# Performance work log

Hardware: AMD Instinct MI355X
Metric: run time of the kernel (lower is better)

The kernel has to match this reference:

```python
import jax, jax.numpy as jnp
import numpy as np

B, S, E = 2, 2048, 2048
H, KV, D = 16, 4, 128
G = H // KV  # query heads per kv head
THETA = 10000.0


def setup_inputs() -> dict:
    key = jax.random.key(0)
    ks = jax.random.split(key, 5)
    scale = 0.02
    return {
        "x": jax.random.normal(ks[0], (B, S, E), dtype=jnp.float32),
        "Wq": jax.random.normal(ks[1], (E, H * D), dtype=jnp.float32) * scale,
        "Wk": jax.random.normal(ks[2], (E, KV * D), dtype=jnp.float32) * scale,
        "Wv": jax.random.normal(ks[3], (E, KV * D), dtype=jnp.float32) * scale,
        "Wo": jax.random.normal(ks[4], (E, E), dtype=jnp.float32) * scale,
    }


def _rope_tables(seq_len, head_dim, theta):
    inv_freq = 1.0 / theta ** (jnp.arange(0, head_dim, 2, dtype=jnp.float32) / head_dim)
    t = jnp.arange(seq_len, dtype=jnp.float32)
    freqs = jnp.outer(t, inv_freq)  # [S, D/2]
    cos = jnp.concatenate([jnp.cos(freqs), jnp.cos(freqs)], axis=-1)  # [S, D]
    sin = jnp.concatenate([jnp.sin(freqs), jnp.sin(freqs)], axis=-1)
    return cos, sin


def _apply_rope(x, cos, sin):
    # x: [B, h, S, D]; cos/sin: [S, D] broadcast over batch/heads
    d2 = x.shape[-1] // 2
    x1, x2 = x[..., :d2], x[..., d2:]
    rotated = jnp.concatenate([-x2, x1], axis=-1)
    return x * cos + rotated * sin


def reference(x, Wq, Wk, Wv, Wo):
    b, s, _ = x.shape
    q = (x @ Wq).reshape(b, s, H, D).transpose(0, 2, 1, 3)   # [B,H,S,D]
    k = (x @ Wk).reshape(b, s, KV, D).transpose(0, 2, 1, 3)  # [B,KV,S,D]
    v = (x @ Wv).reshape(b, s, KV, D).transpose(0, 2, 1, 3)

    cos, sin = _rope_tables(s, D, THETA)
    q = _apply_rope(q, cos, sin)
    k = _apply_rope(k, cos, sin)

    # GQA: q head h attends to kv head h // G (repeat_interleave order)
    qg = q.reshape(b, KV, G, s, D)
    scores = jnp.einsum("bkgsd,bktd->bkgst", qg, k) / jnp.sqrt(jnp.asarray(D, x.dtype))
    causal = jnp.tril(jnp.ones((s, s), dtype=bool))
    scores = jnp.where(causal, scores, jnp.asarray(-jnp.inf, scores.dtype))
    attn = jax.nn.softmax(scores, axis=-1)
    out = jnp.einsum("bkgst,bktd->bkgsd", attn, v)  # [B,KV,G,S,D]
    out = out.reshape(b, H, s, D).transpose(0, 2, 1, 3).reshape(b, s, H * D)
    return out @ Wo
```

## Files before the change

### kernel.cpp

```cpp
#include <hip/hip_runtime.h>
#include <stdint.h>

#define B_ 2
#define S_ 2048
#define E_ 2048
#define H_ 16
#define KV_ 4
#define D_ 128
#define G_ (H_ / KV_)
#define M_ (B_ * S_)
#define NQKV 3072

typedef unsigned short u16;
typedef unsigned int u32;
typedef __bf16 bf16x8 __attribute__((ext_vector_type(8)));
typedef float f32x4 __attribute__((ext_vector_type(4)));

__device__ __forceinline__ u16 f2bf(float f) {
  __bf16 h = (__bf16)f;
  return *(u16*)&h;
}
__device__ __forceinline__ float bf2f(u16 x) {
  return __uint_as_float(((u32)x) << 16);
}

__device__ __forceinline__ void gload_lds16(const u16* g, u16* lds) {
  __builtin_amdgcn_global_load_lds((const __attribute__((address_space(1))) u32*)g,
                                   (__attribute__((address_space(3))) u32*)lds,
                                   16, 0, 0);
}

__global__ __launch_bounds__(256) void build_trig(float2* __restrict__ tbl) {
  int i = blockIdx.x * 256 + threadIdx.x;
  if (i >= S_ * 64) return;
  int d = i & 63, s = i >> 6;
  float ang = (float)s * expf(-0.14391156831212787f * (float)d);
  float sn, cs;
  sincosf(ang, &sn, &cs);
  tbl[i] = make_float2(cs, sn);
}

__global__ __launch_bounds__(256) void convert_fp32_bf16(const float4* __restrict__ x,
                                                         uint2* __restrict__ o, int n4) {
  int i = blockIdx.x * 256 + threadIdx.x;
  if (i >= n4) return;
  float4 v = x[i];
  uint2 r;
  r.x = (u32)f2bf(v.x) | ((u32)f2bf(v.y) << 16);
  r.y = (u32)f2bf(v.z) | ((u32)f2bf(v.w) << 16);
  o[i] = r;
}

__global__ __launch_bounds__(256) void transpose_conv_all(const float* __restrict__ Wq,
                                                          const float* __restrict__ Wk,
                                                          const float* __restrict__ Wv,
                                                          const float* __restrict__ Wo,
                                                          u16* __restrict__ WqT,
                                                          u16* __restrict__ WkT,
                                                          u16* __restrict__ WvT,
                                                          u16* __restrict__ WoT) {
  __shared__ float tile[32][33];
  int bx = blockIdx.x;
  const float* W;
  u16* Wt;
  int Ndim, nx;
  if (bx < 64)       { W = Wq; Wt = WqT; Ndim = 2048; nx = bx; }
  else if (bx < 80)  { W = Wk; Wt = WkT; Ndim = 512;  nx = bx - 64; }
  else if (bx < 96)  { W = Wv; Wt = WvT; Ndim = 512;  nx = bx - 80; }
  else               { W = Wo; Wt = WoT; Ndim = 2048; nx = bx - 96; }
  int n0 = nx * 32, k0 = blockIdx.y * 32;
  int tx = threadIdx.x, ty = threadIdx.y;
#pragma unroll
  for (int i = 0; i < 4; i++) {
    int r = ty + i * 8;
    tile[r][tx] = W[(size_t)(k0 + r) * Ndim + n0 + tx];
  }
  __syncthreads();
#pragma unroll
  for (int i = 0; i < 4; i++) {
    int r = ty + i * 8;
    Wt[(size_t)(n0 + r) * 2048 + k0 + tx] = f2bf(tile[tx][r]);
  }
}

__global__ __launch_bounds__(256) void transpose_v(const u16* __restrict__ QKV,
                                                   u16* __restrict__ Vt) {
  __shared__ u16 tile[32][33];
  int bkv = blockIdx.z;
  int b = bkv / KV_, kv = bkv % KV_;
  int s0 = blockIdx.x * 32, d0 = blockIdx.y * 32;
  int tx = threadIdx.x, ty = threadIdx.y;
#pragma unroll
  for (int i = 0; i < 4; i++) {
    int r = ty + i * 8;
    tile[r][tx] = QKV[(size_t)(b * S_ + s0 + r) * NQKV + 2560 + kv * D_ + d0 + tx];
  }
  __syncthreads();
#pragma unroll
  for (int i = 0; i < 4; i++) {
    int r = ty + i * 8;
    Vt[((size_t)(b * KV_ + kv) * D_ + d0 + r) * S_ + s0 + tx] = tile[tx][r];
  }
}

__global__ __launch_bounds__(256) void rope_k_repack(const u16* __restrict__ QKV,
                                                     u16* __restrict__ Kp,
                                                     const float2* __restrict__ tbl,
                                                     int total) {
  int idx = blockIdx.x * 256 + threadIdx.x;
  if (idx >= total) return;
  int d = idx & 63;
  int rem = idx >> 6;
  int kv = rem & (KV_ - 1);
  int row = rem >> 2;
  int b = row >> 11;
  int spos = row & (S_ - 1);
  size_t src = (size_t)row * NQKV + 2048 + kv * D_ + d;
  float x0 = bf2f(QKV[src]);
  float x1 = bf2f(QKV[src + 64]);
  float2 t = tbl[(spos << 6) + d];
  size_t dst = ((size_t)((b * KV_ + kv) * S_ + spos)) * D_ + d;
  Kp[dst]      = f2bf(x0 * t.x - x1 * t.y);
  Kp[dst + 64] = f2bf(x1 * t.x + x0 * t.y);
}

__global__ __launch_bounds__(256) void rope_q_inplace(u16* __restrict__ QKV,
                                                      const float2* __restrict__ tbl,
                                                      int total) {
  int idx = blockIdx.x * 256 + threadIdx.x;
  if (idx >= total) return;
  int d = idx & 63;
  int rem = idx >> 6;
  int h = rem & (H_ - 1);
  int row = rem >> 4;
  int spos = row & (S_ - 1);
  size_t base = (size_t)row * NQKV + h * D_ + d;
  float x0 = bf2f(QKV[base]);
  float x1 = bf2f(QKV[base + 64]);
  float2 t = tbl[(spos << 6) + d];
  const float scale = 0.08838834764831845f;
  QKV[base]      = f2bf((x0 * t.x - x1 * t.y) * scale);
  QKV[base + 64] = f2bf((x1 * t.x + x0 * t.y) * scale);
}

__global__ __launch_bounds__(512, 2) void gemm256x192_qkv(const u16* __restrict__ A,
                                                          const u16* __restrict__ Bt,
                                                          u16* __restrict__ C) {
  extern __shared__ __align__(16) u16 smem[];
  const int Kdim = 2048;
  const int m0 = blockIdx.y * 256, n0 = blockIdx.x * 192;
  const int tid  = threadIdx.x;
  const int lane = tid & 63;
  const int wave = tid >> 6;
  const int wm   = wave >> 2;
  const int wn   = wave & 3;
  const int quad = lane >> 4, lm = lane & 15;

  int soffA[2], sldbA[2];
#pragma unroll
  for (int i = 0; i < 2; i++) {
    int cc  = i * 512 + tid;
    int row = cc >> 3;
    int q   = (cc & 7) ^ (row & 7);
    soffA[i] = row * Kdim + q * 8;
    sldbA[i] = (i * 512 + wave * 64) * 8;
  }
  const int rowB = tid >> 3;
  const int soffB = rowB * Kdim + (((tid & 7) ^ (rowB & 7)) * 8);
  const int sldbB = wave * 512;
  auto STAGE_A = [&](const u16* g, u16* l) {
    gload_lds16(g + soffA[0], l + sldbA[0]);
    gload_lds16(g + soffA[1], l + sldbA[1]);
  };
  auto STAGE_B = [&](const u16* g, u16* l) {
    gload_lds16(g + soffB, l + sldbB);
  };

  int cs0 = ((0 + quad) ^ (lm & 7)) * 8;
  int cs1 = ((4 + quad) ^ (lm & 7)) * 8;

  const u16* Ag = A  + (size_t)m0 * Kdim;
  const u16* Bg = Bt + (size_t)n0 * Kdim;
  const size_t hstepA = (size_t)128 * Kdim;
  const size_t tstepB = (size_t)64 * Kdim;

  f32x4 acc[8][3];
  f32x4 zero = {0.f, 0.f, 0.f, 0.f};
#pragma unroll
  for (int m = 0; m < 8; m++)
#pragma unroll
    for (int n = 0; n < 3; n++) acc[m][n] = zero;

  int bthird[3], brow[3];
#pragma unroll
  for (int nt = 0; nt < 3; nt++) {
    int R = wn * 48 + nt * 16;
    bthird[nt] = R >> 6;
    brow[nt] = (R & 63) + lm;
  }

  const int NKT = Kdim >> 6;

  STAGE_B(Bg,                    smem + 32768 + 0 * 4096);
  STAGE_A(Ag,                    smem + 0 * 8192);
  STAGE_A(Ag + hstepA,           smem + 1 * 8192);
  STAGE_B(Bg + tstepB,           smem + 32768 + 1 * 4096);
  STAGE_B(Bg + 2 * tstepB,       smem + 32768 + 2 * 4096);
  STAGE_B(Bg + 64,               smem + 32768 + 3 * 4096);
  STAGE_A(Ag + 64,               smem + 2 * 8192);
  STAGE_A(Ag + hstepA + 64,      smem + 3 * 8192);
  asm volatile("s_waitcnt vmcnt(5)" ::: "memory");
  __builtin_amdgcn_s_barrier();

  for (int kt = 0; kt < NKT; ++kt) {
    const int cur = kt & 1;
    const u16* regA  = smem + (cur * 2 + wm) * 8192;
    const u16* regB3 = smem + 32768 + cur * 3 * 4096;
    bf16x8 af[4][2], bf[3][2];

#pragma unroll
    for (int nt = 0; nt < 3; nt++) {
      const u16* p = regB3 + bthird[nt] * 4096 + brow[nt] * 64;
      bf[nt][0] = *(const bf16x8*)(p + cs0);
      bf[nt][1] = *(const bf16x8*)(p + cs1);
    }
#pragma unroll
    for (int m = 0; m < 4; m++) {
      af[m][0] = *(const bf16x8*)(regA + (m * 16 + lm) * 64 + cs0);
      af[m][1] = *(const bf16x8*)(regA + (m * 16 + lm) * 64 + cs1);
    }
    if (kt + 1 < NKT) {
      const u16* bn = Bg + (size_t)(kt + 1) * 64;
      u16* sb = smem + 32768 + ((cur ^ 1) * 3) * 4096;
      STAGE_B(bn + tstepB,     sb + 1 * 4096);
      STAGE_B(bn + 2 * tstepB, sb + 2 * 4096);
    }
    asm volatile("s_waitcnt lgkmcnt(0)" ::: "memory");
    __builtin_amdgcn_s_barrier();
    __builtin_amdgcn_s_setprio(1);
#pragma unroll
    for (int m = 0; m < 4; m++)
#pragma unroll
      for (int n = 0; n < 2; n++) {
        acc[m][n] = __builtin_amdgcn_mfma_f32_16x16x32_bf16(af[m][0], bf[n][0], acc[m][n], 0, 0, 0);
        acc[m][n] = __builtin_amdgcn_mfma_f32_16x16x32_bf16(af[m][1], bf[n][1], acc[m][n], 0, 0, 0);
      }
    __builtin_amdgcn_s_setprio(0);
    __builtin_amdgcn_s_barrier();

    if (kt + 2 < NKT)
      STAGE_B(Bg + (size_t)(kt + 2) * 64, smem + 32768 + (cur * 3 + 0) * 4096);
    __builtin_amdgcn_s_barrier();
    __builtin_amdgcn_s_setprio(1);
#pragma unroll
    for (int m = 0; m < 4; m++) {
      acc[m][2] = __builtin_amdgcn_mfma_f32_16x16x32_bf16(af[m][0], bf[2][0], acc[m][2], 0, 0, 0);
      acc[m][2] = __builtin_amdgcn_mfma_f32_16x16x32_bf16(af[m][1], bf[2][1], acc[m][2], 0, 0, 0);
    }
    __builtin_amdgcn_s_setprio(0);
    __builtin_amdgcn_s_barrier();

#pragma unroll
    for (int m = 0; m < 4; m++) {
      af[m][0] = *(const bf16x8*)(regA + ((m + 4) * 16 + lm) * 64 + cs0);
      af[m][1] = *(const bf16x8*)(regA + ((m + 4) * 16 + lm) * 64 + cs1);
    }
    asm volatile("s_waitcnt lgkmcnt(0)" ::: "memory");
    __builtin_amdgcn_s_barrier();
    __builtin_amdgcn_s_setprio(1);
#pragma unroll
    for (int m = 0; m < 4; m++)
#pragma unroll
      for (int n = 0; n < 2; n++) {
        acc[m + 4][n] = __builtin_amdgcn_mfma_f32_16x16x32_bf16(af[m][0], bf[n][0], acc[m + 4][n], 0, 0, 0);
        acc[m + 4][n] = __builtin_amdgcn_mfma_f32_16x16x32_bf16(af[m][1], bf[n][1], acc[m + 4][n], 0, 0, 0);
      }
    __builtin_amdgcn_s_setprio(0);
    __builtin_amdgcn_s_barrier();

    if (kt + 2 < NKT) {
      STAGE_A(Ag + (size_t)(kt + 2) * 64,          smem + (cur * 2 + 0) * 8192);
      STAGE_A(Ag + hstepA + (size_t)(kt + 2) * 64, smem + (cur * 2 + 1) * 8192);
    }
    __builtin_amdgcn_s_setprio(1);
#pragma unroll
    for (int m = 0; m < 4; m++) {
      acc[m + 4][2] = __builtin_amdgcn_mfma_f32_16x16x32_bf16(af[m][0], bf[2][0], acc[m + 4][2], 0, 0, 0);
      acc[m + 4][2] = __builtin_amdgcn_mfma_f32_16x16x32_bf16(af[m][1], bf[2][1], acc[m + 4][2], 0, 0, 0);
    }
    __builtin_amdgcn_s_setprio(0);
    asm volatile("s_waitcnt vmcnt(5)" ::: "memory");
    __builtin_amdgcn_s_barrier();
  }

#pragma unroll
  for (int m = 0; m < 8; m++) {
    const int row = m0 + wm * 128 + m * 16 + quad * 4;
#pragma unroll
    for (int n = 0; n < 3; n++) {
      const int col = n0 + wn * 48 + n * 16 + lm;
#pragma unroll
      for (int r = 0; r < 4; r++)
        C[(size_t)(row + r) * NQKV + col] = f2bf(acc[m][n][r]);
    }
  }
}

__global__ __launch_bounds__(512, 2) void gemm256x128_wo(const u16* __restrict__ A,
                                                         const u16* __restrict__ Bt,
                                                         float* __restrict__ C) {
  extern __shared__ __align__(16) u16 smem[];
  const int Kdim = 2048, Ndim = 2048;
  const int m0 = blockIdx.y * 256, n0 = blockIdx.x * 128;
  const int tid  = threadIdx.x;
  const int lane = tid & 63;
  const int wave = tid >> 6;
  const int wm   = wave >> 2;
  const int wn   = wave & 3;
  const int bh   = wn >> 1;
  const int nb   = (wn & 1) * 32;
  const int quad = lane >> 4, lm = lane & 15;

  int soffA[2], sldbA[2];
#pragma unroll
  for (int i = 0; i < 2; i++) {
    int cc  = i * 512 + tid;
    int row = cc >> 3;
    int q   = (cc & 7) ^ (row & 7);
    soffA[i] = row * Kdim + q * 8;
    sldbA[i] = (i * 512 + wave * 64) * 8;
  }
  const int rowB = tid >> 3;
  const int soffB = rowB * Kdim + (((tid & 7) ^ (rowB & 7)) * 8);
  const int sldbB = wave * 512;
  auto STAGE_A = [&](const u16* g, u16* l) {
    gload_lds16(g + soffA[0], l + sldbA[0]);
    gload_lds16(g + soffA[1], l + sldbA[1]);
  };
  auto STAGE_B = [&](const u16* g, u16* l) {
    gload_lds16(g + soffB, l + sldbB);
  };

  int cs0 = ((0 + quad) ^ (lm & 7)) * 8;
  int cs1 = ((4 + quad) ^ (lm & 7)) * 8;

  const u16* Ag = A  + (size_t)m0 * Kdim;
  const u16* Bg = Bt + (size_t)n0 * Kdim;
  const size_t hstepA = (size_t)128 * Kdim;
  const size_t hstepB = (size_t)64 * Kdim;

  f32x4 acc[8][2];
  f32x4 zero = {0.f, 0.f, 0.f, 0.f};
#pragma unroll
  for (int m = 0; m < 8; m++) {
    acc[m][0] = zero;
    acc[m][1] = zero;
  }

  const int NKT = Kdim >> 6;

  STAGE_B(Bg,              smem + 32768 + 0 * 4096);
  STAGE_A(Ag,              smem + 0 * 8192);
  STAGE_A(Ag + hstepA,     smem + 1 * 8192);
  STAGE_B(Bg + hstepB,     smem + 32768 + 1 * 4096);
  STAGE_B(Bg + 64,         smem + 32768 + 2 * 4096);
  STAGE_A(Ag + 64,         smem + 2 * 8192);
  STAGE_A(Ag + hstepA + 64, smem + 3 * 8192);
  asm volatile("s_waitcnt vmcnt(5)" ::: "memory");
  __builtin_amdgcn_s_barrier();

  for (int kt = 0; kt < NKT; ++kt) {
    const int cur = kt & 1;
    const u16* regA = smem + (cur * 2 + wm) * 8192;
    const u16* regB = smem + 32768 + (cur * 2 + bh) * 4096;
    bf16x8 af[4][2], bf[2][2];

#pragma unroll
    for (int n = 0; n < 2; n++) {
      bf[n][0] = *(const bf16x8*)(regB + (nb + n * 16 + lm) * 64 + cs0);
      bf[n][1] = *(const bf16x8*)(regB + (nb + n * 16 + lm) * 64 + cs1);
    }
#pragma unroll
    for (int m = 0; m < 4; m++) {
      af[m][0] = *(const bf16x8*)(regA + (m * 16 + lm) * 64 + cs0);
      af[m][1] = *(const bf16x8*)(regA + (m * 16 + lm) * 64 + cs1);
    }
    if (kt + 1 < NKT)
      STAGE_B(Bg + hstepB + (size_t)(kt + 1) * 64,
              smem + 32768 + (((kt + 1) & 1) * 2 + 1) * 4096);
    asm volatile("s_waitcnt lgkmcnt(0)" ::: "memory");
    __builtin_amdgcn_s_barrier();
    __builtin_amdgcn_s_setprio(1);
#pragma unroll
    for (int m = 0; m < 2; m++)
#pragma unroll
      for (int n = 0; n < 2; n++) {
        acc[m][n] = __builtin_amdgcn_mfma_f32_16x16x32_bf16(af[m][0], bf[n][0], acc[m][n], 0, 0, 0);
        acc[m][n] = __builtin_amdgcn_mfma_f32_16x16x32_bf16(af[m][1], bf[n][1], acc[m][n], 0, 0, 0);
      }
    __builtin_amdgcn_s_setprio(0);
    __builtin_amdgcn_s_barrier();

    if (kt + 2 < NKT)
      STAGE_B(Bg + (size_t)(kt + 2) * 64, smem + 32768 + (cur * 2 + 0) * 4096);
    __builtin_amdgcn_s_barrier();
    __builtin_amdgcn_s_setprio(1);
#pragma unroll
    for (int m = 2; m < 4; m++)
#pragma unroll
      for (int n = 0; n < 2; n++) {
        acc[m][n] = __builtin_amdgcn_mfma_f32_16x16x32_bf16(af[m][0], bf[n][0], acc[m][n], 0, 0, 0);
        acc[m][n] = __builtin_amdgcn_mfma_f32_16x16x32_bf16(af[m][1], bf[n][1], acc[m][n], 0, 0, 0);
      }
    __builtin_amdgcn_s_setprio(0);
    __builtin_amdgcn_s_barrier();

#pragma unroll
    for (int m = 0; m < 4; m++) {
      af[m][0] = *(const bf16x8*)(regA + ((m + 4) * 16 + lm) * 64 + cs0);
      af[m][1] = *(const bf16x8*)(regA + ((m + 4) * 16 + lm) * 64 + cs1);
    }
    asm volatile("s_waitcnt lgkmcnt(0)" ::: "memory");
    __builtin_amdgcn_s_barrier();
    __builtin_amdgcn_s_setprio(1);
#pragma unroll
    for (int m = 0; m < 2; m++)
#pragma unroll
      for (int n = 0; n < 2; n++) {
        acc[m + 4][n] = __builtin_amdgcn_mfma_f32_16x16x32_bf16(af[m][0], bf[n][0], acc[m + 4][n], 0, 0, 0);
        acc[m + 4][n] = __builtin_amdgcn_mfma_f32_16x16x32_bf16(af[m][1], bf[n][1], acc[m + 4][n], 0, 0, 0);
      }
    __builtin_amdgcn_s_setprio(0);
    __builtin_amdgcn_s_barrier();

    if (kt + 2 < NKT) {
      STAGE_A(Ag + (size_t)(kt + 2) * 64,          smem + (cur * 2 + 0) * 8192);
      STAGE_A(Ag + hstepA + (size_t)(kt + 2) * 64, smem + (cur * 2 + 1) * 8192);
    }
    __builtin_amdgcn_s_setprio(1);
#pragma unroll
    for (int m = 2; m < 4; m++)
#pragma unroll
      for (int n = 0; n < 2; n++) {
        acc[m + 4][n] = __builtin_amdgcn_mfma_f32_16x16x32_bf16(af[m][0], bf[n][0], acc[m + 4][n], 0, 0, 0);
        acc[m + 4][n] = __builtin_amdgcn_mfma_f32_16x16x32_bf16(af[m][1], bf[n][1], acc[m + 4][n], 0, 0, 0);
      }
    __builtin_amdgcn_s_setprio(0);
    asm volatile("s_waitcnt vmcnt(5)" ::: "memory");
    __builtin_amdgcn_s_barrier();
  }

#pragma unroll
  for (int m = 0; m < 8; m++) {
    const int row = m0 + wm * 128 + m * 16 + quad * 4;
#pragma unroll
    for (int n = 0; n < 2; n++) {
      const int col = n0 + wn * 32 + n * 16 + lm;
#pragma unroll
      for (int r = 0; r < 4; r++)
        C[(size_t)(row + r) * Ndim + col] = acc[m][n][r];
    }
  }
}

__global__ __launch_bounds__(512, 4) void attn_kernel(const u16* __restrict__ Q,
                                                      const u16* __restrict__ Kp,
                                                      const u16* __restrict__ Vt,
                                                      u16* __restrict__ O) {
  __shared__ __align__(16) u16 Ksh[2][64 * 128];
  __shared__ __align__(16) u16 Vsh[128 * 64];
  __shared__ __align__(16) u16 Psh[8][16 * 64];

  const int tid = threadIdx.x;
  const int lane = tid & 63;
  const int wave = tid >> 6;
  const int quad = lane >> 4, lm = lane & 15;
  const int b = blockIdx.z, h = blockIdx.x;
  const int y = blockIdx.y;
  const int kh = h / G_;
  const int qi = b ? y : (15 - y);

  const u16* Kbase = Kp + (size_t)(b * KV_ + kh) * S_ * D_;
  const u16* Vbase = Vt + (size_t)(b * KV_ + kh) * D_ * S_;
  u16* pw = &Psh[wave][0];

  int offK[2], offV[2], ldsOff[2];
#pragma unroll
  for (int i = 0; i < 2; i++) {
    int idx = (wave * 2 + i) * 64 + lane;
    int rK = idx >> 4;
    int cK = (idx & 15) ^ (rK & 7);
    offK[i] = rK * 128 + cK * 8;
    int rV = idx >> 3;
    int cV = (idx & 7) ^ (rV & 7);
    offV[i] = rV * S_ + cV * 8;
    ldsOff[i] = (wave * 2 + i) * 512;
  }

  bf16x8 onesb;
#pragma unroll
  for (int j = 0; j < 8; j++) onesb[j] = (__bf16)1.0f;

  const int sq0 = qi * 128;
  const int nT = 2 * qi + 2;
  const int wrow = sq0 + wave * 16;

  const u16* qptr = Q + (size_t)(b * S_ + wrow + lm) * NQKV + h * D_;
  bf16x8 qf[4];
#pragma unroll
  for (int ks = 0; ks < 4; ks++)
    qf[ks] = *(const bf16x8*)(qptr + ks * 32 + quad * 8);

  f32x4 o[8];
  f32x4 lacc = {0.f, 0.f, 0.f, 0.f};
#pragma unroll
  for (int i = 0; i < 8; i++) o[i] = f32x4{0.f, 0.f, 0.f, 0.f};

#pragma unroll
  for (int i = 0; i < 2; i++)
    gload_lds16(Kbase + offK[i], &Ksh[0][ldsOff[i]]);

  for (int t = 0; t < nT; t++) {
    const int sk0 = t << 6;
    const bool act = (sk0 <= wrow + 15);

    __builtin_amdgcn_s_barrier();

#pragma unroll
    for (int i = 0; i < 2; i++)
      gload_lds16(Vbase + sk0 + offV[i], &Vsh[ldsOff[i]]);
    if (t + 1 < nT) {
      const u16* kg = Kbase + (size_t)(t + 1) * 64 * 128;
      u16* kb_next = &Ksh[(t + 1) & 1][0];
#pragma unroll
      for (int i = 0; i < 2; i++)
        gload_lds16(kg + offK[i], kb_next + ldsOff[i]);
      asm volatile("s_waitcnt vmcnt(4)" ::: "memory");
    } else {
      asm volatile("s_waitcnt vmcnt(2)" ::: "memory");
    }

    __builtin_amdgcn_s_barrier();
    __builtin_amdgcn_sched_barrier(0);

    if (act) {
      const u16* kbuf = &Ksh[t & 1][0];
      f32x4 sc[4];
#pragma unroll
      for (int nt = 0; nt < 4; nt++) sc[nt] = f32x4{0.f, 0.f, 0.f, 0.f};
      __builtin_amdgcn_s_setprio(1);
#pragma unroll
      for (int ks = 0; ks < 4; ks++) {
#pragma unroll
        for (int nt = 0; nt < 4; nt++) {
          int R = nt * 16 + lm;
          bf16x8 kb = *(const bf16x8*)(kbuf + R * 128 + (((ks * 4 + quad) ^ (R & 7)) * 8));
          sc[nt] = __builtin_amdgcn_mfma_f32_16x16x32_bf16(qf[ks], kb, sc[nt], 0, 0, 0);
        }
      }
      __builtin_amdgcn_s_setprio(0);
      const bool nm = (sk0 + 63 > wrow);
#pragma unroll
      for (int nt = 0; nt < 4; nt++)
#pragma unroll
        for (int r = 0; r < 4; r++) {
          float p = __expf(sc[nt][r]);
          if (nm) {
            int kc = sk0 + nt * 16 + lm;
            int qr = wrow + quad * 4 + r;
            p = (kc > qr) ? 0.f : p;
          }
          sc[nt][r] = p;
        }
#pragma unroll
      for (int nt = 0; nt < 4; nt++)
#pragma unroll
        for (int r = 0; r < 4; r++) {
          int p = quad * 4 + r;
          int c = nt * 2 + (lm >> 3);
          pw[p * 64 + ((c ^ (p & 7)) * 8) + (lm & 7)] = f2bf(sc[nt][r]);
        }
    }

    if (t + 1 < nT) {
      asm volatile("s_waitcnt vmcnt(2)" ::: "memory");
    } else {
      asm volatile("s_waitcnt vmcnt(0)" ::: "memory");
    }
    __builtin_amdgcn_s_barrier();
    __builtin_amdgcn_sched_barrier(0);

    if (act) {
      __builtin_amdgcn_s_setprio(1);
#pragma unroll
      for (int ks = 0; ks < 2; ks++) {
        int pr = lm;
        bf16x8 pa = *(const bf16x8*)(pw + pr * 64 + (((ks * 4 + quad) ^ (pr & 7)) * 8));
        lacc = __builtin_amdgcn_mfma_f32_16x16x32_bf16(pa, onesb, lacc, 0, 0, 0);
#pragma unroll
        for (int d8 = 0; d8 < 8; d8++) {
          int R = d8 * 16 + lm;
          bf16x8 vb = *(const bf16x8*)(Vsh + R * 64 + (((ks * 4 + quad) ^ (R & 7)) * 8));
          o[d8] = __builtin_amdgcn_mfma_f32_16x16x32_bf16(pa, vb, o[d8], 0, 0, 0);
        }
      }
      __builtin_amdgcn_s_setprio(0);
    }
  }

  float inv[4];
#pragma unroll
  for (int r = 0; r < 4; r++) inv[r] = 1.0f / lacc[r];
#pragma unroll
  for (int d8 = 0; d8 < 8; d8++)
#pragma unroll
    for (int r = 0; r < 4; r++) {
      int srow = wrow + quad * 4 + r;
      O[((size_t)(b * S_ + srow) * H_ + h) * D_ + d8 * 16 + lm] = f2bf(o[d8][r] * inv[r]);
    }
}

extern "C" void kernel_launch(void* const* d_in, const int* in_sizes, int n_in,
                              void* d_out, int out_size, void* d_ws, size_t ws_size,
                              hipStream_t stream) {
  const float* x  = (const float*)d_in[0];
  const float* Wq = (const float*)d_in[1];
  const float* Wk = (const float*)d_in[2];
  const float* Wv = (const float*)d_in[3];
  const float* Wo = (const float*)d_in[4];
  float* out = (float*)d_out;
  char* ws = (char*)d_ws;
  u16* Xb   = (u16*)(ws);
  u16* Wcat = (u16*)(ws + (16ull << 20));
  u16* WqT  = Wcat;
  u16* WkT  = (u16*)(ws + (24ull << 20));
  u16* WvT  = (u16*)(ws + (26ull << 20));
  u16* WoT  = (u16*)(ws + (28ull << 20));
  u16* QKVb = (u16*)(ws + (36ull << 20));
  u16* Vt   = (u16*)(ws + (60ull << 20));
  u16* Ob   = (u16*)(ws + (64ull << 20));
  u16* Kp   = (u16*)(ws + (80ull << 20));
  float2* trig = (float2*)(ws + (84ull << 20));

  static bool attr_set = false;
  if (!attr_set) {
    hipFuncSetAttribute((const void*)gemm256x192_qkv,
                        hipFuncAttributeMaxDynamicSharedMemorySize, 114688);
    hipFuncSetAttribute((const void*)gemm256x128_wo,
                        hipFuncAttributeMaxDynamicSharedMemorySize, 98304);
    attr_set = true;
  }

  dim3 tb32(32, 8);

  build_trig<<<dim3(S_ * 64 / 256), 256, 0, stream>>>(trig);

  convert_fp32_bf16<<<dim3(M_ * E_ / 4 / 256), 256, 0, stream>>>((const float4*)x, (uint2*)Xb, M_ * E_ / 4);

  transpose_conv_all<<<dim3(160, 64), tb32, 0, stream>>>(Wq, Wk, Wv, Wo, WqT, WkT, WvT, WoT);

  gemm256x192_qkv<<<dim3(16, 16), 512, 114688, stream>>>(Xb, Wcat, QKVb);

  rope_q_inplace<<<dim3(M_ * H_ * 64 / 256), 256, 0, stream>>>(QKVb, trig, M_ * H_ * 64);

  rope_k_repack<<<dim3(M_ * KV_ * 64 / 256), 256, 0, stream>>>(QKVb, Kp, trig, M_ * KV_ * 64);

  transpose_v<<<dim3(S_ / 32, D_ / 32, B_ * KV_), tb32, 0, stream>>>(QKVb, Vt);

  attn_kernel<<<dim3(H_, 16, B_), 512, 0, stream>>>(QKVb, Kp, Vt, Ob);

  gemm256x128_wo<<<dim3(2048 / 128, M_ / 256), 512, 98304, stream>>>(Ob, WoT, out);
}
```

Measured before the change: 279.9 us.

## Fuse Q RoPE into attention load and merge K-rope with V transpose

```diff
diff --git a/kernel.cpp b/kernel.cpp
--- a/kernel.cpp
+++ b/kernel.cpp
@@ -83,64 +83,47 @@
   }
 }
 
-__global__ __launch_bounds__(256) void transpose_v(const u16* __restrict__ QKV,
-                                                   u16* __restrict__ Vt) {
+__global__ __launch_bounds__(256) void rope_k_tv(const u16* __restrict__ QKV,
+                                                 u16* __restrict__ Kp,
+                                                 u16* __restrict__ Vt,
+                                                 const float2* __restrict__ tbl) {
   __shared__ u16 tile[32][33];
-  int bkv = blockIdx.z;
-  int b = bkv / KV_, kv = bkv % KV_;
-  int s0 = blockIdx.x * 32, d0 = blockIdx.y * 32;
-  int tx = threadIdx.x, ty = threadIdx.y;
-#pragma unroll
-  for (int i = 0; i < 4; i++) {
-    int r = ty + i * 8;
-    tile[r][tx] = QKV[(size_t)(b * S_ + s0 + r) * NQKV + 2560 + kv * D_ + d0 + tx];
-  }
-  __syncthreads();
-#pragma unroll
-  for (int i = 0; i < 4; i++) {
-    int r = ty + i * 8;
-    Vt[((size_t)(b * KV_ + kv) * D_ + d0 + r) * S_ + s0 + tx] = tile[tx][r];
-  }
-}
-
-__global__ __launch_bounds__(256) void rope_k_repack(const u16* __restrict__ QKV,
-                                                     u16* __restrict__ Kp,
-                                                     const float2* __restrict__ tbl,
-                                                     int total) {
-  int idx = blockIdx.x * 256 + threadIdx.x;
-  if (idx >= total) return;
-  int d = idx & 63;
-  int rem = idx >> 6;
-  int kv = rem & (KV_ - 1);
-  int row = rem >> 2;
-  int b = row >> 11;
-  int spos = row & (S_ - 1);
-  size_t src = (size_t)row * NQKV + 2048 + kv * D_ + d;
-  float x0 = bf2f(QKV[src]);
-  float x1 = bf2f(QKV[src + 64]);
-  float2 t = tbl[(spos << 6) + d];
-  size_t dst = ((size_t)((b * KV_ + kv) * S_ + spos)) * D_ + d;
-  Kp[dst]      = f2bf(x0 * t.x - x1 * t.y);
-  Kp[dst + 64] = f2bf(x1 * t.x + x0 * t.y);
-}
-
-__global__ __launch_bounds__(256) void rope_q_inplace(u16* __restrict__ QKV,
-                                                      const float2* __restrict__ tbl,
-                                                      int total) {
-  int idx = blockIdx.x * 256 + threadIdx.x;
-  if (idx >= total) return;
-  int d = idx & 63;
-  int rem = idx >> 6;
-  int h = rem & (H_ - 1);
-  int row = rem >> 4;
-  int spos = row & (S_ - 1);
-  size_t base = (size_t)row * NQKV + h * D_ + d;
-  float x0 = bf2f(QKV[base]);
-  float x1 = bf2f(QKV[base + 64]);
-  float2 t = tbl[(spos << 6) + d];
-  const float scale = 0.08838834764831845f;
-  QKV[base]      = f2bf((x0 * t.x - x1 * t.y) * scale);
-  QKV[base + 64] = f2bf((x1 * t.x + x0 * t.y) * scale);
+  int bx = blockIdx.x;
+  int tid = threadIdx.x;
+  if (bx < 4096) {
+    int idx = bx * 256 + tid;
+    int d = idx & 63;
+    int rem = idx >> 6;
+    int kv = rem & (KV_ - 1);
+    int row = rem >> 2;
+    int b = row >> 11;
+    int spos = row & (S_ - 1);
+    size_t src = (size_t)row * NQKV + 2048 + kv * D_ + d;
+    float x0 = bf2f(QKV[src]);
+    float x1 = bf2f(QKV[src + 64]);
+    float2 t = tbl[(spos << 6) + d];
+    size_t dst = ((size_t)((b * KV_ + kv) * S_ + spos)) * D_ + d;
+    Kp[dst]      = f2bf(x0 * t.x - x1 * t.y);
+    Kp[dst + 64] = f2bf(x1 * t.x + x0 * t.y);
+  } else {
+    int i = bx - 4096;
+    int s0 = (i & 63) * 32;
+    int d0 = ((i >> 6) & 3) * 32;
+    int bkv = i >> 8;
+    int b = bkv / KV_, kv = bkv % KV_;
+    int tx = tid & 31, ty = tid >> 5;
+#pragma unroll
+    for (int k = 0; k < 4; k++) {
+      int r = ty + k * 8;
+      tile[r][tx] = QKV[(size_t)(b * S_ + s0 + r) * NQKV + 2560 + kv * D_ + d0 + tx];
+    }
+    __syncthreads();
+#pragma unroll
+    for (int k = 0; k < 4; k++) {
+      int r = ty + k * 8;
+      Vt[((size_t)(b * KV_ + kv) * D_ + d0 + r) * S_ + s0 + tx] = tile[tx][r];
+    }
+  }
 }
 
 __global__ __launch_bounds__(512, 2) void gemm256x192_qkv(const u16* __restrict__ A,
@@ -466,7 +449,8 @@
 __global__ __launch_bounds__(512, 4) void attn_kernel(const u16* __restrict__ Q,
                                                       const u16* __restrict__ Kp,
                                                       const u16* __restrict__ Vt,
-                                                      u16* __restrict__ O) {
+                                                      u16* __restrict__ O,
+                                                      const float2* __restrict__ tbl) {
   __shared__ __align__(16) u16 Ksh[2][64 * 128];
   __shared__ __align__(16) u16 Vsh[128 * 64];
   __shared__ __align__(16) u16 Psh[8][16 * 64];
@@ -505,11 +489,23 @@
   const int nT = 2 * qi + 2;
   const int wrow = sq0 + wave * 16;
 
-  const u16* qptr = Q + (size_t)(b * S_ + wrow + lm) * NQKV + h * D_;
+  const int spos = wrow + lm;
+  const u16* qptr = Q + (size_t)(b * S_ + spos) * NQKV + h * D_;
   bf16x8 qf[4];
 #pragma unroll
-  for (int ks = 0; ks < 4; ks++)
-    qf[ks] = *(const bf16x8*)(qptr + ks * 32 + quad * 8);
+  for (int ks = 0; ks < 2; ks++) {
+    bf16x8 a = *(const bf16x8*)(qptr + ks * 32 + quad * 8);
+    bf16x8 c = *(const bf16x8*)(qptr + (ks + 2) * 32 + quad * 8);
+#pragma unroll
+    for (int j = 0; j < 8; j++) {
+      int d = ks * 32 + quad * 8 + j;
+      float2 t = tbl[(spos << 6) + d];
+      float x0 = (float)a[j], x1 = (float)c[j];
+      const float scale = 0.08838834764831845f;
+      qf[ks][j]     = (__bf16)((x0 * t.x - x1 * t.y) * scale);
+      qf[ks + 2][j] = (__bf16)((x1 * t.x + x0 * t.y) * scale);
+    }
+  }
 
   f32x4 o[8];
   f32x4 lacc = {0.f, 0.f, 0.f, 0.f};
@@ -661,13 +657,9 @@
 
   gemm256x192_qkv<<<dim3(16, 16), 512, 114688, stream>>>(Xb, Wcat, QKVb);
 
-  rope_q_inplace<<<dim3(M_ * H_ * 64 / 256), 256, 0, stream>>>(QKVb, trig, M_ * H_ * 64);
-
-  rope_k_repack<<<dim3(M_ * KV_ * 64 / 256), 256, 0, stream>>>(QKVb, Kp, trig, M_ * KV_ * 64);
-
-  transpose_v<<<dim3(S_ / 32, D_ / 32, B_ * KV_), tb32, 0, stream>>>(QKVb, Vt);
-
-  attn_kernel<<<dim3(H_, 16, B_), 512, 0, stream>>>(QKVb, Kp, Vt, Ob);
+  rope_k_tv<<<dim3(4096 + 2048), 256, 0, stream>>>(QKVb, Kp, Vt, trig);
+
+  attn_kernel<<<dim3(H_, 16, B_), 512, 0, stream>>>(QKVb, Kp, Vt, Ob, trig);
 
   gemm256x128_wo<<<dim3(2048 / 128, M_ / 256), 512, 98304, stream>>>(Ob, WoT, out);
 }
```

After: 274.4 us. 2.0% less time.
